# Kernel tuning notes

Measured on AMD Instinct MI355X. Metric: run time of the kernel, lower is better.

The kernel has to match this reference:

```python
import jax, jax.numpy as jnp
import numpy as np

N_USERS = 100000
M_ITEMS = 50000
EMBED = 64
N_LAYERS = 3
NNZ = 2400000
BATCH = 8192


def setup_inputs() -> dict:
    key = jax.random.key(0)
    ks = jax.random.split(key, 8)
    user = jax.random.randint(ks[0], (BATCH,), 0, N_USERS)
    item_i = jax.random.randint(ks[1], (BATCH,), 0, M_ITEMS)
    item_j = jax.random.randint(ks[2], (BATCH,), 0, M_ITEMS)
    timestamp = jax.random.uniform(ks[3], (BATCH,), dtype=jnp.float32)
    # symmetric bipartite edge list: user->item and item->user halves
    half = NNZ // 2
    u = jax.random.randint(ks[4], (half,), 0, N_USERS)
    it = jax.random.randint(ks[5], (half,), 0, M_ITEMS) + N_USERS
    edge_src = jnp.concatenate([u, it])
    edge_dst = jnp.concatenate([it, u])
    v = jax.random.uniform(ks[6], (half,), dtype=jnp.float32)
    edge_vals = jnp.concatenate([v, v])  # symmetric normalized weights
    embed_user_0 = jax.random.normal(ks[7], (N_USERS, EMBED), dtype=jnp.float32) * 0.1
    embed_item_0 = jax.random.normal(jax.random.fold_in(key, 99), (M_ITEMS, EMBED), dtype=jnp.float32) * 0.1
    return {
        'user': user, 'item_i': item_i, 'item_j': item_j,
        'timestamp': timestamp, 'split_idx': 0,
        'edge_src': edge_src, 'edge_dst': edge_dst, 'edge_vals': edge_vals,
        'embed_user_0': embed_user_0, 'embed_item_0': embed_item_0,
    }


def reference(user, item_i, item_j, timestamp, split_idx,
              edge_src, edge_dst, edge_vals, embed_user_0, embed_item_0):
    N = N_USERS + M_ITEMS
    # LightGCN propagation: mean over layer-0..n_layers embeddings
    all_emb = jnp.concatenate([embed_user_0, embed_item_0], axis=0)  # [N, D]
    emb = all_emb
    emb_sum = all_emb
    for _ in range(N_LAYERS):
        # sparse.mm(Graph, emb): gather source features along edges, scale, segment-reduce
        emb = jax.ops.segment_sum(edge_vals[:, None] * emb[edge_dst], edge_src,
                                  num_segments=N)
        emb_sum = emb_sum + emb
    light_out = emb_sum / (N_LAYERS + 1)
    embed_user = light_out[:N_USERS]
    embed_item = light_out[N_USERS:]

    ue = embed_user[user]          # [B, D]
    ie = embed_item[item_i]        # [B, D]
    je = embed_item[item_j]        # [B, D]
    prediction_i = jnp.sum(ue * ie, axis=-1)
    prediction_j = jnp.sum(ue * je, axis=-1)

    # reg_loss uses layer-0 embeddings gathered at the batch indices
    u0 = embed_user_0[user]
    i0 = embed_item_0[item_i]
    j0 = embed_item_0[item_j]
    reg_loss = 0.5 * (jnp.sum(u0 * u0) + jnp.sum(i0 * i0) + jnp.sum(j0 * j0)) / user.shape[0]
    return prediction_i, prediction_j, reg_loss
```

## Files before the change

### kernel.cpp

```cpp
#include <hip/hip_runtime.h>
#include <hip/hip_fp16.h>

#define N_USERS 100000
#define M_ITEMS 50000
#define NNODES  (N_USERS + M_ITEMS)
#define EMBED   64
#define BATCH   8192

#define NU_E ((size_t)N_USERS * EMBED)
#define NE   ((size_t)NNODES * EMBED)

#define SBN    512
#define NSB    ((NNODES + SBN - 1) / SBN)
#define CAP    14336
#define CSTR   16
#define PBLK   512
#define PTILE  4688
#define PRED_BLOCKS ((BATCH * 64) / 256)

typedef unsigned int uint;

static __device__ __forceinline__ ushort f2bf(float f) {
    uint u = __float_as_uint(f);
    return (ushort)((u + 0x7fffu + ((u >> 16) & 1u)) >> 16);
}
static __device__ __forceinline__ float bf_lo(uint u) { return __uint_as_float(u << 16); }
static __device__ __forceinline__ float bf_hi(uint u) { return __uint_as_float(u & 0xffff0000u); }
static __device__ __forceinline__ float bfs(ushort u) { return __uint_as_float((uint)u << 16); }

static __device__ __forceinline__ int packe(int d, int fbits) {
    ushort h = __half_as_ushort(__float2half(__int_as_float(fbits)));
    return (int)(((uint)d << 15) | (uint)(h & 0x7fffu));
}
static __device__ __forceinline__ float unp_val(int p) {
    return __half2float(__ushort_as_half((ushort)(p & 0x7fff)));
}

__global__ void init_all(const float* __restrict__ eu, const float* __restrict__ ei,
                         ushort* __restrict__ E0, int* __restrict__ gcur) {
    if (blockIdx.x == 0) {
        for (int i = threadIdx.x; i < NSB; i += 1024) gcur[i * CSTR] = i * CAP;
        return;
    }
    size_t t = (size_t)(blockIdx.x - 1) * 1024 + threadIdx.x;
    const size_t nu4 = NU_E / 4;
    const size_t n4  = NE / 4;
    if (t >= n4) return;
    float4 v = (t < nu4) ? ((const float4*)eu)[t] : ((const float4*)ei)[t - nu4];
    ((ushort4*)E0)[t] = make_ushort4(f2bf(v.x), f2bf(v.y), f2bf(v.z), f2bf(v.w));
}

__global__ void __launch_bounds__(1024)
partition2(const int* __restrict__ src, const int* __restrict__ dst,
           const float* __restrict__ vals, int* __restrict__ gcur,
           int2* __restrict__ ebuf, int nnz) {
    __shared__ int2 data[PTILE];
    __shared__ int  cnt[NSB];
    __shared__ int  cur[NSB];
    __shared__ int  lbeg[NSB];
    __shared__ int  gbase[NSB];
    __shared__ int  wsum[16];
    const int blk = blockIdx.x;
    const int tid = threadIdx.x;
    const int lane = tid & 63, w = tid >> 6;
    const int base = blk * PTILE;
    const int end  = min(base + PTILE, nnz);

    for (int i = tid; i < NSB; i += 1024) cnt[i] = 0;
    __syncthreads();
    for (int i = base + tid; i < end; i += 1024)
        atomicAdd(&cnt[src[i] >> 9], 1);
    __syncthreads();
    int c = (tid < NSB) ? cnt[tid] : 0;
    int v = c;
    #pragma unroll
    for (int off = 1; off < 64; off <<= 1) {
        int t = __shfl_up(v, off);
        if (lane >= off) v += t;
    }
    if (lane == 63) wsum[w] = v;
    __syncthreads();
    int wpre = 0;
    #pragma unroll
    for (int k = 0; k < 16; ++k) wpre += (k < w) ? wsum[k] : 0;
    v += wpre;
    if (tid < NSB) {
        int ex = v - c;
        cur[tid]  = ex;
        lbeg[tid] = ex;
        if (c > 0) gbase[tid] = atomicAdd(&gcur[tid * CSTR], c);
    }
    __syncthreads();
    for (int i = base + tid; i < end; i += 1024) {
        int sv = src[i];
        int d  = dst[i];
        float fv = vals[i];
        if (d >= N_USERS) d -= N_USERS;
        int p = atomicAdd(&cur[sv >> 9], 1);
        data[p] = make_int2((sv & 511) | (d << 9), __float_as_int(fv));
    }
    __syncthreads();
    int grp = tid >> 4, lane16 = tid & 15;
    for (int b = grp; b < NSB; b += 64) {
        int cc = cnt[b];
        if (cc == 0) continue;
        int lb = lbeg[b];
        int gb = gbase[b];
        for (int j = lane16; j < cc; j += 16)
            ebuf[gb + j] = data[lb + j];
    }
}

__global__ void __launch_bounds__(1024)
sb_sort(const int* __restrict__ gcur, const int2* __restrict__ ebuf,
        int2* __restrict__ offs2, int* __restrict__ ep,
        int* __restrict__ perm) {
    __shared__ int cnt[SBN], cur[SBN], bcnt[256];
    __shared__ int wsum[16];
    int sb  = blockIdx.x;
    int tid = threadIdx.x;
    int lane = tid & 63, w = tid >> 6;
    int beg = sb * CAP;
    int end = gcur[sb * CSTR];
    if (tid < SBN) cnt[tid] = 0;
    __syncthreads();
    for (int i = beg + tid; i < end; i += 1024)
        atomicAdd(&cnt[ebuf[i].x & (SBN - 1)], 1);
    __syncthreads();
    int c = (tid < SBN) ? cnt[tid] : 0;
    int v = c;
    #pragma unroll
    for (int off = 1; off < 64; off <<= 1) {
        int t = __shfl_up(v, off);
        if (lane >= off) v += t;
    }
    if (lane == 63) wsum[w] = v;
    __syncthreads();
    if (tid < SBN) {
        int wpre = 0;
        #pragma unroll
        for (int k = 0; k < 8; ++k) wpre += (k < w) ? wsum[k] : 0;
        v += wpre;
        int lbase = v - c;
        int node = sb * SBN + tid;
        if (node < NNODES) offs2[node] = make_int2(beg + lbase, c);
        cur[tid] = lbase;
    }
    __syncthreads();
    for (int i = beg + tid; i < end; i += 1024) {
        int2 e = ebuf[i];
        int p = atomicAdd(&cur[e.x & (SBN - 1)], 1);
        ep[beg + p] = packe(e.x >> 9, e.y);
    }
    __syncthreads();
    if (tid < 256) bcnt[tid] = 0;
    __syncthreads();
    int nodeCount = min(NNODES - sb * SBN, SBN);
    int bin = 0;
    if (tid < nodeCount) {
        bin = 255 - min(cnt[tid], 255);
        atomicAdd(&bcnt[bin], 1);
    }
    __syncthreads();
    int c2 = (tid < 256) ? bcnt[tid] : 0;
    int v2 = c2;
    #pragma unroll
    for (int off = 1; off < 64; off <<= 1) {
        int t = __shfl_up(v2, off);
        if (lane >= off) v2 += t;
    }
    if (tid < 256 && lane == 63) wsum[w] = v2;
    __syncthreads();
    if (tid < 256) {
        int wpre = 0;
        #pragma unroll
        for (int k = 0; k < 4; ++k) wpre += (k < w) ? wsum[k] : 0;
        v2 += wpre;
        cur[tid] = sb * SBN + (v2 - c2);
    }
    __syncthreads();
    if (tid < nodeCount) {
        int rank = atomicAdd(&cur[bin], 1);
        perm[rank] = sb * SBN + tid;
    }
}

__global__ void gather_E(const int2* __restrict__ offs2, const int* __restrict__ ep,
                         const int* __restrict__ perm,
                         const ushort* __restrict__ Eprev, ushort* __restrict__ Enext) {
    int t = blockIdx.x * blockDim.x + threadIdx.x;
    int wave = t >> 6;
    int lane = t & 63;
    int g = lane >> 3;
    int q = lane & 7;
    int ln = wave * 8 + g;
    bool valid = ln < NNODES;
    int node = valid ? perm[ln] : 0;
    int2 od = valid ? offs2[node] : make_int2(0, 0);
    int start = od.x;
    int deg   = od.y;
    const uint4* other = (const uint4*)(Eprev + (node < N_USERS ? NU_E : 0));
    int lastIdx = max(start + deg - 1, 0);

    int md = deg;
    #pragma unroll
    for (int off = 8; off <= 32; off <<= 1) md = max(md, __shfl_xor(md, off));

    float a0=0.f,a1=0.f,a2=0.f,a3=0.f,a4=0.f,a5=0.f,a6=0.f,a7=0.f;
    for (int k = 0; k < md; k += 16) {
        int e[16];
        uint4 r[16];
        #pragma unroll
        for (int c = 0; c < 16; ++c) {
            int idx = (k + c < deg) ? start + k + c : lastIdx;
            e[c] = ep[idx];
            if (k + c >= deg) e[c] = 0;
        }
        #pragma unroll
        for (int c = 0; c < 16; ++c)
            r[c] = other[(size_t)(((uint)e[c]) >> 15) * 8 + q];
        #pragma unroll
        for (int c = 0; c < 16; ++c) {
            float v = unp_val(e[c]);
            a0 = fmaf(v, bf_lo(r[c].x), a0);  a1 = fmaf(v, bf_hi(r[c].x), a1);
            a2 = fmaf(v, bf_lo(r[c].y), a2);  a3 = fmaf(v, bf_hi(r[c].y), a3);
            a4 = fmaf(v, bf_lo(r[c].z), a4);  a5 = fmaf(v, bf_hi(r[c].z), a5);
            a6 = fmaf(v, bf_lo(r[c].w), a6);  a7 = fmaf(v, bf_hi(r[c].w), a7);
        }
    }

    if (!valid) return;
    uint4 o;
    o.x = (uint)f2bf(a0) | ((uint)f2bf(a1) << 16);
    o.y = (uint)f2bf(a2) | ((uint)f2bf(a3) << 16);
    o.z = (uint)f2bf(a4) | ((uint)f2bf(a5) << 16);
    o.w = (uint)f2bf(a6) | ((uint)f2bf(a7) << 16);
    ((uint4*)Enext)[(size_t)node * 8 + q] = o;
}

__global__ void predict_kernel(const int* __restrict__ user, const int* __restrict__ item_i,
                               const int* __restrict__ item_j,
                               const ushort* __restrict__ E0, const ushort* __restrict__ E1,
                               const ushort* __restrict__ E2, const ushort* __restrict__ E3,
                               const float* __restrict__ eu0, const float* __restrict__ ei0,
                               float* __restrict__ out, float* __restrict__ rbuf) {
    __shared__ float rpart[4];
    int t = blockIdx.x * blockDim.x + threadIdx.x;
    int b = t >> 6;
    int d = t & 63;
    int wv = threadIdx.x >> 6;
    float pi = 0.f, pj = 0.f, r = 0.f;
    if (b < BATCH) {
        size_t ru = (size_t)user[b] * EMBED + d;
        size_t ri = ((size_t)N_USERS + item_i[b]) * EMBED + d;
        size_t rj = ((size_t)N_USERS + item_j[b]) * EMBED + d;
        float ue = bfs(E0[ru]) + bfs(E1[ru]) + bfs(E2[ru]) + bfs(E3[ru]);
        float ie = bfs(E0[ri]) + bfs(E1[ri]) + bfs(E2[ri]) + bfs(E3[ri]);
        float je = bfs(E0[rj]) + bfs(E1[rj]) + bfs(E2[rj]) + bfs(E3[rj]);
        pi = ue * ie;
        pj = ue * je;
        float u0 = eu0[(size_t)user[b] * EMBED + d];
        float i0 = ei0[(size_t)item_i[b] * EMBED + d];
        float j0 = ei0[(size_t)item_j[b] * EMBED + d];
        r = u0 * u0 + i0 * i0 + j0 * j0;
    }
    #pragma unroll
    for (int off = 32; off > 0; off >>= 1) {
        pi += __shfl_down(pi, off);
        pj += __shfl_down(pj, off);
        r  += __shfl_down(r,  off);
    }
    if (d == 0 && b < BATCH) {
        out[b]         = pi * (1.0f / 16.0f);
        out[BATCH + b] = pj * (1.0f / 16.0f);
        rpart[wv] = r;
    }
    __syncthreads();
    if (threadIdx.x == 0)
        rbuf[blockIdx.x] = rpart[0] + rpart[1] + rpart[2] + rpart[3];
}

__global__ void finalize_reg(const float* __restrict__ rbuf, float* __restrict__ out) {
    __shared__ float lds[4];
    int tid = threadIdx.x;
    float s = 0.f;
    for (int i = tid; i < PRED_BLOCKS; i += 256) s += rbuf[i];
    #pragma unroll
    for (int off = 32; off > 0; off >>= 1) s += __shfl_down(s, off);
    if ((tid & 63) == 0) lds[tid >> 6] = s;
    __syncthreads();
    if (tid == 0)
        out[2 * BATCH] = (lds[0] + lds[1] + lds[2] + lds[3]) * (0.5f / (float)BATCH);
}

extern "C" void kernel_launch(void* const* d_in, const int* in_sizes, int n_in,
                              void* d_out, int out_size, void* d_ws, size_t ws_size,
                              hipStream_t stream) {
    const int*   user      = (const int*)  d_in[0];
    const int*   item_i    = (const int*)  d_in[1];
    const int*   item_j    = (const int*)  d_in[2];
    const int*   edge_src  = (const int*)  d_in[5];
    const int*   edge_dst  = (const int*)  d_in[6];
    const float* edge_vals = (const float*)d_in[7];
    const float* eu0       = (const float*)d_in[8];
    const float* ei0       = (const float*)d_in[9];
    const int    nnz       = in_sizes[5];

    float* out = (float*)d_out;

    ushort* E0    = (ushort*)d_ws;
    ushort* E1    = E0 + NE;
    ushort* E2    = E1 + NE;
    ushort* E3    = E2 + NE;
    int*    ep    = (int*)(E3 + NE);
    int2*   offs2 = (int2*)(ep + (size_t)NSB * CAP);
    int*    gcur  = (int*)(offs2 + NNODES);
    int*    perm  = gcur + NSB * CSTR;
    float*  rbuf  = (float*)(perm + NNODES);
    int2*   ebuf  = (int2*)E1;

    const int initBlocks = (int)((NE / 4 + 1023) / 1024);

    init_all<<<1 + initBlocks, 1024, 0, stream>>>(eu0, ei0, E0, gcur);
    partition2<<<PBLK, 1024, 0, stream>>>(edge_src, edge_dst, edge_vals,
                                          gcur, ebuf, nnz);
    sb_sort<<<NSB, 1024, 0, stream>>>(gcur, ebuf, offs2, ep, perm);
    const int gblocks = (int)((((NNODES + 7) / 8) * 64 + 255) / 256);
    gather_E<<<gblocks, 256, 0, stream>>>(offs2, ep, perm, E0, E1);
    gather_E<<<gblocks, 256, 0, stream>>>(offs2, ep, perm, E1, E2);
    gather_E<<<gblocks, 256, 0, stream>>>(offs2, ep, perm, E2, E3);
    predict_kernel<<<PRED_BLOCKS, 256, 0, stream>>>(
        user, item_i, item_j, E0, E1, E2, E3, eu0, ei0, out, rbuf);
    finalize_reg<<<1, 256, 0, stream>>>(rbuf, out);
}
```

Before: 307.8 us.

## Compute final propagation layer only for nodes referenced by the batch

Marks the user and item nodes that appear in the batch, compacts them into a list during the sort kernel, and runs the third-layer gather only over those nodes instead of all 150k. This removes most of the last layer's gather traffic, since predictions need E3 only at batch indices. It adds a memset, a marking pass and atomic list compaction, and it assumes the number of distinct marked users and items stays within the fixed MAXU and MAXI caps.

```diff
diff --git a/kernel.cpp b/kernel.cpp
--- a/kernel.cpp
+++ b/kernel.cpp
@@ -17,6 +17,10 @@
 #define PBLK   512
 #define PTILE  4688
 #define PRED_BLOCKS ((BATCH * 64) / 256)
+#define MAXU   8192
+#define MAXI   16384
+#define NLSLOT (MAXU + MAXI)
+#define CBLK   37
 
 typedef unsigned int uint;
 
@@ -37,12 +41,26 @@
 }
 
 __global__ void init_all(const float* __restrict__ eu, const float* __restrict__ ei,
-                         ushort* __restrict__ E0, int* __restrict__ gcur) {
+                         ushort* __restrict__ E0, int* __restrict__ gcur,
+                         int* __restrict__ cpt, char* __restrict__ mark,
+                         const int* __restrict__ user, const int* __restrict__ item_i,
+                         const int* __restrict__ item_j) {
     if (blockIdx.x == 0) {
         for (int i = threadIdx.x; i < NSB; i += 1024) gcur[i * CSTR] = i * CAP;
+        if (threadIdx.x < 2) cpt[threadIdx.x] = 0;
         return;
     }
-    size_t t = (size_t)(blockIdx.x - 1) * 1024 + threadIdx.x;
+    if (blockIdx.x == 1) {
+        for (int j = threadIdx.x; j < 3 * BATCH; j += 1024) {
+            int which = j >> 13;
+            int b = j & (BATCH - 1);
+            int node = (which == 0) ? user[b]
+                     : N_USERS + ((which == 1) ? item_i[b] : item_j[b]);
+            mark[node] = 1;
+        }
+        return;
+    }
+    size_t t = (size_t)(blockIdx.x - 2) * 1024 + threadIdx.x;
     const size_t nu4 = NU_E / 4;
     const size_t n4  = NE / 4;
     if (t >= n4) return;
@@ -114,11 +132,30 @@
 __global__ void __launch_bounds__(1024)
 sb_sort(const int* __restrict__ gcur, const int2* __restrict__ ebuf,
         int2* __restrict__ offs2, int* __restrict__ ep,
-        int* __restrict__ perm) {
+        int* __restrict__ perm,
+        const char* __restrict__ mark, int* __restrict__ nlist,
+        int* __restrict__ cpt) {
+    int tid = threadIdx.x;
+    if (blockIdx.x >= NSB) {
+        int cb = blockIdx.x - NSB;
+        #pragma unroll
+        for (int j = 0; j < 4; ++j) {
+            int i = cb * 4096 + j * 1024 + tid;
+            if (i < NNODES && mark[i]) {
+                if (i < N_USERS) {
+                    int p = atomicAdd(&cpt[0], 1);
+                    nlist[p] = i;
+                } else {
+                    int p = atomicAdd(&cpt[1], 1);
+                    nlist[MAXU + p] = i;
+                }
+            }
+        }
+        return;
+    }
     __shared__ int cnt[SBN], cur[SBN], bcnt[256];
     __shared__ int wsum[16];
     int sb  = blockIdx.x;
-    int tid = threadIdx.x;
     int lane = tid & 63, w = tid >> 6;
     int beg = sb * CAP;
     int end = gcur[sb * CSTR];
@@ -196,6 +233,62 @@
     int ln = wave * 8 + g;
     bool valid = ln < NNODES;
     int node = valid ? perm[ln] : 0;
+    int2 od = valid ? offs2[node] : make_int2(0, 0);
+    int start = od.x;
+    int deg   = od.y;
+    const uint4* other = (const uint4*)(Eprev + (node < N_USERS ? NU_E : 0));
+    int lastIdx = max(start + deg - 1, 0);
+
+    int md = deg;
+    #pragma unroll
+    for (int off = 8; off <= 32; off <<= 1) md = max(md, __shfl_xor(md, off));
+
+    float a0=0.f,a1=0.f,a2=0.f,a3=0.f,a4=0.f,a5=0.f,a6=0.f,a7=0.f;
+    for (int k = 0; k < md; k += 16) {
+        int e[16];
+        uint4 r[16];
+        #pragma unroll
+        for (int c = 0; c < 16; ++c) {
+            int idx = (k + c < deg) ? start + k + c : lastIdx;
+            e[c] = ep[idx];
+            if (k + c >= deg) e[c] = 0;
+        }
+        #pragma unroll
+        for (int c = 0; c < 16; ++c)
+            r[c] = other[(size_t)(((uint)e[c]) >> 15) * 8 + q];
+        #pragma unroll
+        for (int c = 0; c < 16; ++c) {
+            float v = unp_val(e[c]);
+            a0 = fmaf(v, bf_lo(r[c].x), a0);  a1 = fmaf(v, bf_hi(r[c].x), a1);
+            a2 = fmaf(v, bf_lo(r[c].y), a2);  a3 = fmaf(v, bf_hi(r[c].y), a3);
+            a4 = fmaf(v, bf_lo(r[c].z), a4);  a5 = fmaf(v, bf_hi(r[c].z), a5);
+            a6 = fmaf(v, bf_lo(r[c].w), a6);  a7 = fmaf(v, bf_hi(r[c].w), a7);
+        }
+    }
+
+    if (!valid) return;
+    uint4 o;
+    o.x = (uint)f2bf(a0) | ((uint)f2bf(a1) << 16);
+    o.y = (uint)f2bf(a2) | ((uint)f2bf(a3) << 16);
+    o.z = (uint)f2bf(a4) | ((uint)f2bf(a5) << 16);
+    o.w = (uint)f2bf(a6) | ((uint)f2bf(a7) << 16);
+    ((uint4*)Enext)[(size_t)node * 8 + q] = o;
+}
+
+__global__ void gather_E_list(const int2* __restrict__ offs2, const int* __restrict__ ep,
+                              const int* __restrict__ nlist, const int* __restrict__ cpt,
+                              const ushort* __restrict__ Eprev, ushort* __restrict__ Enext) {
+    int t = blockIdx.x * blockDim.x + threadIdx.x;
+    int wave = t >> 6;
+    int lane = t & 63;
+    int g = lane >> 3;
+    int q = lane & 7;
+    int ln = wave * 8 + g;
+    int cntU = cpt[0], cntI = cpt[1];
+    bool isU = ln < MAXU;
+    int li = isU ? ln : ln - MAXU;
+    bool valid = li < (isU ? cntU : cntI);
+    int node = valid ? nlist[(isU ? 0 : MAXU) + li] : 0;
     int2 od = valid ? offs2[node] : make_int2(0, 0);
     int start = od.x;
     int deg   = od.y;
@@ -317,18 +410,25 @@
     int*    gcur  = (int*)(offs2 + NNODES);
     int*    perm  = gcur + NSB * CSTR;
     float*  rbuf  = (float*)(perm + NNODES);
+    int*    nlist = (int*)(rbuf + PRED_BLOCKS);
+    int*    cpt   = nlist + NLSLOT;
+    char*   mark  = (char*)(cpt + 16);
     int2*   ebuf  = (int2*)E1;
 
     const int initBlocks = (int)((NE / 4 + 1023) / 1024);
 
-    init_all<<<1 + initBlocks, 1024, 0, stream>>>(eu0, ei0, E0, gcur);
+    hipMemsetAsync(mark, 0, NNODES, stream);
+    init_all<<<2 + initBlocks, 1024, 0, stream>>>(eu0, ei0, E0, gcur, cpt, mark,
+                                                  user, item_i, item_j);
     partition2<<<PBLK, 1024, 0, stream>>>(edge_src, edge_dst, edge_vals,
                                           gcur, ebuf, nnz);
-    sb_sort<<<NSB, 1024, 0, stream>>>(gcur, ebuf, offs2, ep, perm);
+    sb_sort<<<NSB + CBLK, 1024, 0, stream>>>(gcur, ebuf, offs2, ep, perm,
+                                             mark, nlist, cpt);
     const int gblocks = (int)((((NNODES + 7) / 8) * 64 + 255) / 256);
     gather_E<<<gblocks, 256, 0, stream>>>(offs2, ep, perm, E0, E1);
     gather_E<<<gblocks, 256, 0, stream>>>(offs2, ep, perm, E1, E2);
-    gather_E<<<gblocks, 256, 0, stream>>>(offs2, ep, perm, E2, E3);
+    const int lblocks = (NLSLOT / 8 * 64) / 256;
+    gather_E_list<<<lblocks, 256, 0, stream>>>(offs2, ep, nlist, cpt, E2, E3);
     predict_kernel<<<PRED_BLOCKS, 256, 0, stream>>>(
         user, item_i, item_j, E0, E1, E2, E3, eu0, ei0, out, rbuf);
     finalize_reg<<<1, 256, 0, stream>>>(rbuf, out);
```

Result: slower. 326.5 us (+6.1%).

## Compute final propagation layer only for batch-referenced nodes

Applied to the files above, without the earlier changes.

The third propagation layer is now computed only for the 3*BATCH user/item nodes the prediction reads, through a new gather_E_list kernel, instead of for all 150k nodes. This removes most of the last layer's gather traffic, since only E3 rows at batch indices are consumed. Duplicate indices are recomputed redundantly and may be written concurrently with identical values. E3 rows for nodes outside the batch are left stale, which is acceptable only because nothing else reads them.

```diff
diff --git a/kernel.cpp b/kernel.cpp
--- a/kernel.cpp
+++ b/kernel.cpp
@@ -230,6 +230,61 @@
     }
 
     if (!valid) return;
+    uint4 o;
+    o.x = (uint)f2bf(a0) | ((uint)f2bf(a1) << 16);
+    o.y = (uint)f2bf(a2) | ((uint)f2bf(a3) << 16);
+    o.z = (uint)f2bf(a4) | ((uint)f2bf(a5) << 16);
+    o.w = (uint)f2bf(a6) | ((uint)f2bf(a7) << 16);
+    ((uint4*)Enext)[(size_t)node * 8 + q] = o;
+}
+
+__global__ void gather_E_list(const int2* __restrict__ offs2, const int* __restrict__ ep,
+                              const int* __restrict__ user, const int* __restrict__ item_i,
+                              const int* __restrict__ item_j,
+                              const ushort* __restrict__ Eprev, ushort* __restrict__ Enext) {
+    int t = blockIdx.x * blockDim.x + threadIdx.x;
+    int wave = t >> 6;
+    int lane = t & 63;
+    int g = lane >> 3;
+    int q = lane & 7;
+    int ln = wave * 8 + g;
+    int b = ln & (BATCH - 1);
+    int which = ln >> 13;
+    int node = (which == 0) ? user[b]
+             : N_USERS + ((which == 1) ? item_i[b] : item_j[b]);
+    int2 od = offs2[node];
+    int start = od.x;
+    int deg   = od.y;
+    const uint4* other = (const uint4*)(Eprev + (node < N_USERS ? NU_E : 0));
+    int lastIdx = max(start + deg - 1, 0);
+
+    int md = deg;
+    #pragma unroll
+    for (int off = 8; off <= 32; off <<= 1) md = max(md, __shfl_xor(md, off));
+
+    float a0=0.f,a1=0.f,a2=0.f,a3=0.f,a4=0.f,a5=0.f,a6=0.f,a7=0.f;
+    for (int k = 0; k < md; k += 16) {
+        int e[16];
+        uint4 r[16];
+        #pragma unroll
+        for (int c = 0; c < 16; ++c) {
+            int idx = (k + c < deg) ? start + k + c : lastIdx;
+            e[c] = ep[idx];
+            if (k + c >= deg) e[c] = 0;
+        }
+        #pragma unroll
+        for (int c = 0; c < 16; ++c)
+            r[c] = other[(size_t)(((uint)e[c]) >> 15) * 8 + q];
+        #pragma unroll
+        for (int c = 0; c < 16; ++c) {
+            float v = unp_val(e[c]);
+            a0 = fmaf(v, bf_lo(r[c].x), a0);  a1 = fmaf(v, bf_hi(r[c].x), a1);
+            a2 = fmaf(v, bf_lo(r[c].y), a2);  a3 = fmaf(v, bf_hi(r[c].y), a3);
+            a4 = fmaf(v, bf_lo(r[c].z), a4);  a5 = fmaf(v, bf_hi(r[c].z), a5);
+            a6 = fmaf(v, bf_lo(r[c].w), a6);  a7 = fmaf(v, bf_hi(r[c].w), a7);
+        }
+    }
+
     uint4 o;
     o.x = (uint)f2bf(a0) | ((uint)f2bf(a1) << 16);
     o.y = (uint)f2bf(a2) | ((uint)f2bf(a3) << 16);
@@ -328,7 +383,9 @@
     const int gblocks = (int)((((NNODES + 7) / 8) * 64 + 255) / 256);
     gather_E<<<gblocks, 256, 0, stream>>>(offs2, ep, perm, E0, E1);
     gather_E<<<gblocks, 256, 0, stream>>>(offs2, ep, perm, E1, E2);
-    gather_E<<<gblocks, 256, 0, stream>>>(offs2, ep, perm, E2, E3);
+    const int lblocks = (3 * BATCH * 8) / 256;
+    gather_E_list<<<lblocks, 256, 0, stream>>>(offs2, ep, user, item_i, item_j,
+                                               E2, E3);
     predict_kernel<<<PRED_BLOCKS, 256, 0, stream>>>(
         user, item_i, item_j, E0, E1, E2, E3, eu0, ei0, out, rbuf);
     finalize_reg<<<1, 256, 0, stream>>>(rbuf, out);
```

Result: faster. 275.0 us (median of 2 runs) (-10.7%).

## Fuse propagation layers into persistent kernel and compute last layer only for batch nodes

Applied to the files above, without the earlier changes.

Replaces the three gather launches plus the predict and finalize kernels with one persistent kernel that uses a software grid barrier between two full propagation layers. The third layer is no longer computed for all nodes; it is evaluated on demand only for the user and item rows referenced by the batch, fused into the prediction. The reg loss is reduced with a global atomic instead of a separate kernel. This cuts launch overhead and skips most of the last layer's gather work. In exchange it relies on all blocks being co-resident for the spin barrier and does a per-dimension, uncoalesced gather for batch rows.

```diff
diff --git a/kernel.cpp b/kernel.cpp
--- a/kernel.cpp
+++ b/kernel.cpp
@@ -16,7 +16,6 @@
 #define CSTR   16
 #define PBLK   512
 #define PTILE  4688
-#define PRED_BLOCKS ((BATCH * 64) / 256)
 
 typedef unsigned int uint;
 
@@ -24,9 +23,9 @@
     uint u = __float_as_uint(f);
     return (ushort)((u + 0x7fffu + ((u >> 16) & 1u)) >> 16);
 }
+static __device__ __forceinline__ float bfs(ushort u) { return __uint_as_float((uint)u << 16); }
 static __device__ __forceinline__ float bf_lo(uint u) { return __uint_as_float(u << 16); }
 static __device__ __forceinline__ float bf_hi(uint u) { return __uint_as_float(u & 0xffff0000u); }
-static __device__ __forceinline__ float bfs(ushort u) { return __uint_as_float((uint)u << 16); }
 
 static __device__ __forceinline__ int packe(int d, int fbits) {
     ushort h = __half_as_ushort(__float2half(__int_as_float(fbits)));
@@ -37,9 +36,11 @@
 }
 
 __global__ void init_all(const float* __restrict__ eu, const float* __restrict__ ei,
-                         ushort* __restrict__ E0, int* __restrict__ gcur) {
+                         ushort* __restrict__ E0, int* __restrict__ gcur,
+                         int* __restrict__ bar, float* __restrict__ facc) {
     if (blockIdx.x == 0) {
         for (int i = threadIdx.x; i < NSB; i += 1024) gcur[i * CSTR] = i * CAP;
+        if (threadIdx.x == 0) { bar[0] = 0; facc[0] = 0.f; }
         return;
     }
     size_t t = (size_t)(blockIdx.x - 1) * 1024 + threadIdx.x;
@@ -185,112 +186,155 @@
     }
 }
 
-__global__ void gather_E(const int2* __restrict__ offs2, const int* __restrict__ ep,
-                         const int* __restrict__ perm,
-                         const ushort* __restrict__ Eprev, ushort* __restrict__ Enext) {
-    int t = blockIdx.x * blockDim.x + threadIdx.x;
-    int wave = t >> 6;
-    int lane = t & 63;
-    int g = lane >> 3;
-    int q = lane & 7;
-    int ln = wave * 8 + g;
-    bool valid = ln < NNODES;
-    int node = valid ? perm[ln] : 0;
-    int2 od = valid ? offs2[node] : make_int2(0, 0);
-    int start = od.x;
-    int deg   = od.y;
-    const uint4* other = (const uint4*)(Eprev + (node < N_USERS ? NU_E : 0));
-    int lastIdx = max(start + deg - 1, 0);
-
-    int md = deg;
-    #pragma unroll
-    for (int off = 8; off <= 32; off <<= 1) md = max(md, __shfl_xor(md, off));
-
-    float a0=0.f,a1=0.f,a2=0.f,a3=0.f,a4=0.f,a5=0.f,a6=0.f,a7=0.f;
-    for (int k = 0; k < md; k += 16) {
-        int e[16];
-        uint4 r[16];
-        #pragma unroll
-        for (int c = 0; c < 16; ++c) {
-            int idx = (k + c < deg) ? start + k + c : lastIdx;
-            e[c] = ep[idx];
-            if (k + c >= deg) e[c] = 0;
-        }
-        #pragma unroll
-        for (int c = 0; c < 16; ++c)
-            r[c] = other[(size_t)(((uint)e[c]) >> 15) * 8 + q];
-        #pragma unroll
-        for (int c = 0; c < 16; ++c) {
-            float v = unp_val(e[c]);
-            a0 = fmaf(v, bf_lo(r[c].x), a0);  a1 = fmaf(v, bf_hi(r[c].x), a1);
-            a2 = fmaf(v, bf_lo(r[c].y), a2);  a3 = fmaf(v, bf_hi(r[c].y), a3);
-            a4 = fmaf(v, bf_lo(r[c].z), a4);  a5 = fmaf(v, bf_hi(r[c].z), a5);
-            a6 = fmaf(v, bf_lo(r[c].w), a6);  a7 = fmaf(v, bf_hi(r[c].w), a7);
-        }
-    }
-
-    if (!valid) return;
-    uint4 o;
-    o.x = (uint)f2bf(a0) | ((uint)f2bf(a1) << 16);
-    o.y = (uint)f2bf(a2) | ((uint)f2bf(a3) << 16);
-    o.z = (uint)f2bf(a4) | ((uint)f2bf(a5) << 16);
-    o.w = (uint)f2bf(a6) | ((uint)f2bf(a7) << 16);
-    ((uint4*)Enext)[(size_t)node * 8 + q] = o;
-}
-
-__global__ void predict_kernel(const int* __restrict__ user, const int* __restrict__ item_i,
-                               const int* __restrict__ item_j,
-                               const ushort* __restrict__ E0, const ushort* __restrict__ E1,
-                               const ushort* __restrict__ E2, const ushort* __restrict__ E3,
-                               const float* __restrict__ eu0, const float* __restrict__ ei0,
-                               float* __restrict__ out, float* __restrict__ rbuf) {
+static __device__ __forceinline__ void gsync(int* bar, int* gen, int nblk) {
+    __syncthreads();
+    if (threadIdx.x == 0) {
+        __threadfence();
+        int g = __hip_atomic_load(gen, __ATOMIC_RELAXED, __HIP_MEMORY_SCOPE_AGENT);
+        int t = __hip_atomic_fetch_add(bar, 1, __ATOMIC_ACQ_REL, __HIP_MEMORY_SCOPE_AGENT);
+        if (t == nblk - 1) {
+            __hip_atomic_store(bar, 0, __ATOMIC_RELAXED, __HIP_MEMORY_SCOPE_AGENT);
+            __hip_atomic_fetch_add(gen, 1, __ATOMIC_RELEASE, __HIP_MEMORY_SCOPE_AGENT);
+        } else {
+            while (__hip_atomic_load(gen, __ATOMIC_ACQUIRE, __HIP_MEMORY_SCOPE_AGENT) == g)
+                __builtin_amdgcn_s_sleep(2);
+        }
+        __threadfence();
+    }
+    __syncthreads();
+}
+
+static __device__ __forceinline__ void gather_phase(
+        const int2* offs2, const int* ep, const int* perm,
+        const ushort* Eprev, ushort* Enext, int gwid, int gw) {
+    int lane = threadIdx.x & 63;
+    int g = lane >> 3, q = lane & 7;
+    for (int base = gwid * 8; base < NNODES; base += gw * 8) {
+        int ln = base + g;
+        bool valid = ln < NNODES;
+        int node = valid ? perm[ln] : 0;
+        int2 od = valid ? offs2[node] : make_int2(0, 0);
+        int start = od.x, deg = od.y;
+        const uint4* other = (const uint4*)(Eprev + (node < N_USERS ? NU_E : 0));
+        int lastIdx = max(start + deg - 1, 0);
+
+        int md = deg;
+        #pragma unroll
+        for (int off = 8; off <= 32; off <<= 1) md = max(md, __shfl_xor(md, off));
+
+        float a0=0.f,a1=0.f,a2=0.f,a3=0.f,a4=0.f,a5=0.f,a6=0.f,a7=0.f;
+        for (int k = 0; k < md; k += 16) {
+            int e[16];
+            uint4 r[16];
+            #pragma unroll
+            for (int c = 0; c < 16; ++c) {
+                int idx = (k + c < deg) ? start + k + c : lastIdx;
+                e[c] = ep[idx];
+                if (k + c >= deg) e[c] = 0;
+            }
+            #pragma unroll
+            for (int c = 0; c < 16; ++c)
+                r[c] = other[(size_t)(((uint)e[c]) >> 15) * 8 + q];
+            #pragma unroll
+            for (int c = 0; c < 16; ++c) {
+                float v = unp_val(e[c]);
+                a0 = fmaf(v, bf_lo(r[c].x), a0);  a1 = fmaf(v, bf_hi(r[c].x), a1);
+                a2 = fmaf(v, bf_lo(r[c].y), a2);  a3 = fmaf(v, bf_hi(r[c].y), a3);
+                a4 = fmaf(v, bf_lo(r[c].z), a4);  a5 = fmaf(v, bf_hi(r[c].z), a5);
+                a6 = fmaf(v, bf_lo(r[c].w), a6);  a7 = fmaf(v, bf_hi(r[c].w), a7);
+            }
+        }
+        if (valid) {
+            uint4 o;
+            o.x = (uint)f2bf(a0) | ((uint)f2bf(a1) << 16);
+            o.y = (uint)f2bf(a2) | ((uint)f2bf(a3) << 16);
+            o.z = (uint)f2bf(a4) | ((uint)f2bf(a5) << 16);
+            o.w = (uint)f2bf(a6) | ((uint)f2bf(a7) << 16);
+            ((uint4*)Enext)[(size_t)node * 8 + q] = o;
+        }
+    }
+}
+
+static __device__ __forceinline__ float grow(int node, const int2* offs2,
+                                             const int* ep, const ushort* E2, int d) {
+    int2 od = offs2[node];
+    int start = od.x, deg = od.y;
+    const ushort* ob = E2 + (node < N_USERS ? NU_E : 0);
+    float a = 0.f;
+    for (int k = 0; k < deg; k += 8) {
+        int e[8];
+        #pragma unroll
+        for (int c = 0; c < 8; ++c)
+            e[c] = (k + c < deg) ? ep[start + k + c] : 0;
+        #pragma unroll
+        for (int c = 0; c < 8; ++c) {
+            ushort rv = ob[(size_t)(((uint)e[c]) >> 15) * 64 + d];
+            a = fmaf(unp_val(e[c]), bfs(rv), a);
+        }
+    }
+    return a;
+}
+
+__global__ void __launch_bounds__(256, 4)
+fused_tail(const int2* offs2, const int* ep, const int* perm,
+           const ushort* E0, ushort* E1, ushort* E2,
+           const int* user, const int* item_i, const int* item_j,
+           const float* eu0, const float* ei0,
+           float* out, int* bar, int* gen, float* facc) {
     __shared__ float rpart[4];
-    int t = blockIdx.x * blockDim.x + threadIdx.x;
-    int b = t >> 6;
-    int d = t & 63;
-    int wv = threadIdx.x >> 6;
-    float pi = 0.f, pj = 0.f, r = 0.f;
-    if (b < BATCH) {
-        size_t ru = (size_t)user[b] * EMBED + d;
-        size_t ri = ((size_t)N_USERS + item_i[b]) * EMBED + d;
-        size_t rj = ((size_t)N_USERS + item_j[b]) * EMBED + d;
-        float ue = bfs(E0[ru]) + bfs(E1[ru]) + bfs(E2[ru]) + bfs(E3[ru]);
-        float ie = bfs(E0[ri]) + bfs(E1[ri]) + bfs(E2[ri]) + bfs(E3[ri]);
-        float je = bfs(E0[rj]) + bfs(E1[rj]) + bfs(E2[rj]) + bfs(E3[rj]);
-        pi = ue * ie;
-        pj = ue * je;
-        float u0 = eu0[(size_t)user[b] * EMBED + d];
-        float i0 = ei0[(size_t)item_i[b] * EMBED + d];
-        float j0 = ei0[(size_t)item_j[b] * EMBED + d];
-        r = u0 * u0 + i0 * i0 + j0 * j0;
-    }
-    #pragma unroll
-    for (int off = 32; off > 0; off >>= 1) {
-        pi += __shfl_down(pi, off);
-        pj += __shfl_down(pj, off);
-        r  += __shfl_down(r,  off);
-    }
-    if (d == 0 && b < BATCH) {
-        out[b]         = pi * (1.0f / 16.0f);
-        out[BATCH + b] = pj * (1.0f / 16.0f);
-        rpart[wv] = r;
-    }
-    __syncthreads();
-    if (threadIdx.x == 0)
-        rbuf[blockIdx.x] = rpart[0] + rpart[1] + rpart[2] + rpart[3];
-}
-
-__global__ void finalize_reg(const float* __restrict__ rbuf, float* __restrict__ out) {
-    __shared__ float lds[4];
-    int tid = threadIdx.x;
-    float s = 0.f;
-    for (int i = tid; i < PRED_BLOCKS; i += 256) s += rbuf[i];
-    #pragma unroll
-    for (int off = 32; off > 0; off >>= 1) s += __shfl_down(s, off);
-    if ((tid & 63) == 0) lds[tid >> 6] = s;
-    __syncthreads();
-    if (tid == 0)
-        out[2 * BATCH] = (lds[0] + lds[1] + lds[2] + lds[3]) * (0.5f / (float)BATCH);
+    const int nblk = gridDim.x;
+    const int gw   = nblk * 4;
+    const int gwid = (blockIdx.x * 256 + threadIdx.x) >> 6;
+    const int lane = threadIdx.x & 63;
+    const int wv   = threadIdx.x >> 6;
+
+    gather_phase(offs2, ep, perm, E0, E1, gwid, gw);
+    gsync(bar, gen, nblk);
+    gather_phase(offs2, ep, perm, E1, E2, gwid, gw);
+    gsync(bar, gen, nblk);
+
+    const int d = lane;
+    float rloc = 0.f;
+    for (int b = gwid; b < BATCH; b += gw) {
+        int u  = user[b];
+        int iv = item_i[b], jv = item_j[b];
+        int ni = N_USERS + iv, nj = N_USERS + jv;
+        float u3 = grow(u,  offs2, ep, E2, d);
+        float i3 = grow(ni, offs2, ep, E2, d);
+        float j3 = grow(nj, offs2, ep, E2, d);
+        size_t ru = (size_t)u  * EMBED + d;
+        size_t ri = (size_t)ni * EMBED + d;
+        size_t rj = (size_t)nj * EMBED + d;
+        float ue = bfs(E0[ru]) + bfs(E1[ru]) + bfs(E2[ru]) + u3;
+        float ie = bfs(E0[ri]) + bfs(E1[ri]) + bfs(E2[ri]) + i3;
+        float je = bfs(E0[rj]) + bfs(E1[rj]) + bfs(E2[rj]) + j3;
+        float pi = ue * ie, pj = ue * je;
+        float u0 = eu0[(size_t)u  * EMBED + d];
+        float i0 = ei0[(size_t)iv * EMBED + d];
+        float j0 = ei0[(size_t)jv * EMBED + d];
+        float r = u0 * u0 + i0 * i0 + j0 * j0;
+        #pragma unroll
+        for (int off = 32; off > 0; off >>= 1) {
+            pi += __shfl_down(pi, off);
+            pj += __shfl_down(pj, off);
+            r  += __shfl_down(r,  off);
+        }
+        if (lane == 0) {
+            out[b]         = pi * (1.0f / 16.0f);
+            out[BATCH + b] = pj * (1.0f / 16.0f);
+            rloc += r;
+        }
+    }
+    if (lane == 0) rpart[wv] = rloc;
+    __syncthreads();
+    if (threadIdx.x == 0) {
+        float s = rpart[0] + rpart[1] + rpart[2] + rpart[3];
+        __hip_atomic_fetch_add(facc, s, __ATOMIC_RELAXED, __HIP_MEMORY_SCOPE_AGENT);
+        int t = __hip_atomic_fetch_add(bar, 1, __ATOMIC_ACQ_REL, __HIP_MEMORY_SCOPE_AGENT);
+        if (t == nblk - 1)
+            out[2 * BATCH] = __hip_atomic_load(facc, __ATOMIC_RELAXED,
+                                               __HIP_MEMORY_SCOPE_AGENT) * (0.5f / (float)BATCH);
+    }
 }
 
 extern "C" void kernel_launch(void* const* d_in, const int* in_sizes, int n_in,
@@ -308,28 +352,36 @@
 
     float* out = (float*)d_out;
 
+    static int NB = 0;
+    if (NB == 0) {
+        hipDeviceProp_t prop;
+        int dev = 0;
+        hipGetDevice(&dev);
+        if (hipGetDeviceProperties(&prop, dev) == hipSuccess && prop.multiProcessorCount > 0)
+            NB = prop.multiProcessorCount * 3;
+        else
+            NB = 768;
+    }
+
     ushort* E0    = (ushort*)d_ws;
     ushort* E1    = E0 + NE;
     ushort* E2    = E1 + NE;
-    ushort* E3    = E2 + NE;
-    int*    ep    = (int*)(E3 + NE);
+    int*    ep    = (int*)(E2 + NE);
     int2*   offs2 = (int2*)(ep + (size_t)NSB * CAP);
     int*    gcur  = (int*)(offs2 + NNODES);
     int*    perm  = gcur + NSB * CSTR;
-    float*  rbuf  = (float*)(perm + NNODES);
+    int*    bar   = perm + NNODES;
+    int*    gen   = bar + 1;
+    float*  facc  = (float*)(gen + 1);
     int2*   ebuf  = (int2*)E1;
 
     const int initBlocks = (int)((NE / 4 + 1023) / 1024);
 
-    init_all<<<1 + initBlocks, 1024, 0, stream>>>(eu0, ei0, E0, gcur);
+    init_all<<<1 + initBlocks, 1024, 0, stream>>>(eu0, ei0, E0, gcur, bar, facc);
     partition2<<<PBLK, 1024, 0, stream>>>(edge_src, edge_dst, edge_vals,
                                           gcur, ebuf, nnz);
     sb_sort<<<NSB, 1024, 0, stream>>>(gcur, ebuf, offs2, ep, perm);
-    const int gblocks = (int)((((NNODES + 7) / 8) * 64 + 255) / 256);
-    gather_E<<<gblocks, 256, 0, stream>>>(offs2, ep, perm, E0, E1);
-    gather_E<<<gblocks, 256, 0, stream>>>(offs2, ep, perm, E1, E2);
-    gather_E<<<gblocks, 256, 0, stream>>>(offs2, ep, perm, E2, E3);
-    predict_kernel<<<PRED_BLOCKS, 256, 0, stream>>>(
-        user, item_i, item_j, E0, E1, E2, E3, eu0, ei0, out, rbuf);
-    finalize_reg<<<1, 256, 0, stream>>>(rbuf, out);
-}
+    fused_tail<<<NB, 256, 0, stream>>>(offs2, ep, perm, E0, E1, E2,
+                                       user, item_i, item_j, eu0, ei0,
+                                       out, bar, gen, facc);
+}
```

Result: slower. 721.2 us (+134.3%).
